# Performance work log

Measured on AMD Instinct MI355X. Metric: run time of the kernel, lower is better.

Reference implementation:

```python
import jax, jax.numpy as jnp
import numpy as np

NH, NP, C = 12, 4, 768           # heads, points, d_model
HD = C // NH                      # head dim (deform_ratio=1.0)
SHAPES = np.array([[128, 128], [64, 64], [32, 32]], dtype=np.int64)
LSI = np.array([0, 128 * 128, 128 * 128 + 64 * 64], dtype=np.int64)
L = SHAPES.shape[0]
EPS = 1e-6


def setup_inputs() -> dict:
    key = jax.random.key(0)
    ks = jax.random.split(key, 10)
    N, Lq = 4, 64 * 64
    Lin = int((SHAPES[:, 0] * SHAPES[:, 1]).sum())
    s = 0.02
    return {
        "query": jax.random.normal(ks[0], (N, Lq, C), jnp.float32),
        "reference_points": jax.random.uniform(ks[1], (N, Lq, L, 2), dtype=jnp.float32),
        "feat": jax.random.normal(ks[2], (N, Lin, C), jnp.float32),
        "qnorm_w": jnp.ones((C,), jnp.float32),
        "qnorm_b": jnp.zeros((C,), jnp.float32),
        "fnorm_w": jnp.ones((C,), jnp.float32),
        "fnorm_b": jnp.zeros((C,), jnp.float32),
        "gamma": jnp.full((C,), 0.01, jnp.float32),
        "so_w": s * jax.random.normal(ks[3], (C, NH * L * NP * 2), jnp.float32),
        "so_b": s * jax.random.normal(ks[4], (NH * L * NP * 2,), jnp.float32),
        "aw_w": s * jax.random.normal(ks[5], (C, NH * L * NP), jnp.float32),
        "aw_b": s * jax.random.normal(ks[6], (NH * L * NP,), jnp.float32),
        "vp_w": s * jax.random.normal(ks[7], (C, C), jnp.float32),
        "vp_b": jnp.zeros((C,), jnp.float32),
        "op_w": s * jax.random.normal(ks[8], (C, C), jnp.float32),
        "op_b": jnp.zeros((C,), jnp.float32),
        "spatial_shapes": SHAPES,
        "level_start_index": LSI,
    }


def _ln(x, w, b):
    mu = x.mean(-1, keepdims=True)
    var = ((x - mu) ** 2).mean(-1, keepdims=True)
    return (x - mu) * jax.lax.rsqrt(var + EPS) * w + b


def reference(query, reference_points, feat, qnorm_w, qnorm_b, fnorm_w, fnorm_b,
              gamma, so_w, so_b, aw_w, aw_b, vp_w, vp_b, op_w, op_b,
              spatial_shapes, level_start_index):
    N, Lq, C_ = query.shape
    ss = np.asarray(spatial_shapes)
    lsi = np.asarray(level_start_index)
    q = _ln(query, qnorm_w, qnorm_b)
    f = _ln(feat, fnorm_w, fnorm_b)
    # value projection -> [N, nh, Lin, hd]
    value = (f @ vp_w + vp_b).reshape(N, -1, NH, HD).transpose(0, 2, 1, 3)
    off = (q @ so_w + so_b).reshape(N, Lq, NH, L, NP, 2)
    aw = jax.nn.softmax((q @ aw_w + aw_b).reshape(N, Lq, NH, L * NP), axis=-1)
    aw = aw.reshape(N, Lq, NH, L, NP)
    # offset normalizer is (W, H) per level
    offset_norm = jnp.asarray(ss[:, ::-1].copy(), jnp.float32)
    loc = reference_points[:, :, None, :, None, :] + off / offset_norm[None, None, None, :, None, :]
    out = jnp.zeros((N, Lq, NH, HD), query.dtype)
    for l in range(L):
        H_, W_ = int(ss[l, 0]), int(ss[l, 1])
        st = int(lsi[l])
        v = value[:, :, st:st + H_ * W_, :]                     # [N,nh,HW,hd]
        ll = loc[:, :, :, l].transpose(0, 2, 1, 3, 4).reshape(N, NH, Lq * NP, 2)
        # grid_sample, align_corners=False: map [0,1] -> pixel coords
        px = ll[..., 0] * W_ - 0.5
        py = ll[..., 1] * H_ - 0.5
        x0 = jnp.floor(px)
        y0 = jnp.floor(py)
        tx = px - x0
        ty = py - y0
        x0i = x0.astype(jnp.int32)
        y0i = y0.astype(jnp.int32)
        acc = jnp.zeros((N, NH, Lq * NP, HD), query.dtype)
        for dx, dy, w in ((0, 0, (1 - tx) * (1 - ty)), (1, 0, tx * (1 - ty)),
                          (0, 1, (1 - tx) * ty), (1, 1, tx * ty)):
            xi = x0i + dx
            yi = y0i + dy
            ok = (xi >= 0) & (xi < W_) & (yi >= 0) & (yi < H_)  # zero padding
            idx = jnp.clip(yi, 0, H_ - 1) * W_ + jnp.clip(xi, 0, W_ - 1)
            g = jnp.take_along_axis(v, idx[..., None], axis=2)   # [N,nh,Lq*P,hd]
            acc = acc + g * (w * ok)[..., None]
        samp = acc.reshape(N, NH, Lq, NP, HD)
        out = out + jnp.einsum('nhqpd,nqhp->nqhd', samp, aw[:, :, :, l])
    attn = out.reshape(N, Lq, C_) @ op_w + op_b
    return query + gamma * attn
```

## Files before the change

### kernel.cpp

```cpp
#include <hip/hip_runtime.h>
#include <hip/hip_bf16.h>
#include <stdint.h>

#define NHD   12
#define NPT   4
#define CDIM  768
#define HDIM  64
#define NLVL  3
#define LQ    4096
#define NB    4
#define LIN   21504
#define MQ    (NB*LQ)
#define MF    (NB*LIN)
#define CAT_N 512
#define AW_OFF 288
#define WSCL  16.f
#define PREP_NB 1537

typedef float  f32x4  __attribute__((ext_vector_type(4)));
typedef float  f32x2  __attribute__((ext_vector_type(2)));
typedef float  f32x16 __attribute__((ext_vector_type(16)));
typedef int    i32x8  __attribute__((ext_vector_type(8)));

__device__ __forceinline__ i32x8 mk8(uint4 lo, uint4 hi) {
  i32x8 v;
  v[0] = (int)lo.x; v[1] = (int)lo.y; v[2] = (int)lo.z; v[3] = (int)lo.w;
  v[4] = (int)hi.x; v[5] = (int)hi.y; v[6] = (int)hi.z; v[7] = (int)hi.w;
  return v;
}

__global__ __launch_bounds__(256) void prep_and_ln(
    const float* __restrict__ vp_w, const float* __restrict__ op_w,
    const float* __restrict__ so_w, const float* __restrict__ aw_w,
    const float* __restrict__ so_b, const float* __restrict__ aw_b,
    char* __restrict__ vp_w8, char* __restrict__ op_w8,
    char* __restrict__ cat_w8, float* __restrict__ cat_bp,
    const float* __restrict__ xq, const float* __restrict__ wq,
    const float* __restrict__ bq, char* __restrict__ yq,
    const float* __restrict__ xf, const float* __restrict__ wf,
    const float* __restrict__ bf, char* __restrict__ yf)
{
  const int blk = blockIdx.x;
  if (blk >= PREP_NB) {
    const int lb = blk - PREP_NB;
    const float* x; const float* w; const float* b; char* y; int row;
    if (lb < MQ / 4) {
      x = xq; w = wq; b = bq; y = yq;
      row = lb * 4 + (threadIdx.x >> 6);
    } else {
      x = xf; w = wf; b = bf; y = yf;
      row = (lb - MQ / 4) * 4 + (threadIdx.x >> 6);
    }
    const int lane = threadIdx.x & 63;
    const float4* xr = (const float4*)(x + (size_t)row * CDIM);
    float4 v[3];
    v[0] = xr[lane]; v[1] = xr[lane + 64]; v[2] = xr[lane + 128];
    float s1 = 0.f, s2 = 0.f;
#pragma unroll
    for (int i = 0; i < 3; ++i) {
      s1 += v[i].x + v[i].y + v[i].z + v[i].w;
      s2 += v[i].x*v[i].x + v[i].y*v[i].y + v[i].z*v[i].z + v[i].w*v[i].w;
    }
#pragma unroll
    for (int o = 32; o > 0; o >>= 1) { s1 += __shfl_xor(s1, o); s2 += __shfl_xor(s2, o); }
    const float mu = s1 * (1.f / CDIM);
    const float rs = rsqrtf(s2 * (1.f / CDIM) - mu * mu + 1e-6f);
#pragma unroll
    for (int i = 0; i < 3; ++i) {
      const float4 w4 = ((const float4*)w)[lane + i * 64];
      const float4 b4 = ((const float4*)b)[lane + i * 64];
      const float o0 = (v[i].x - mu) * rs * w4.x + b4.x;
      const float o1 = (v[i].y - mu) * rs * w4.y + b4.y;
      const float o2 = (v[i].z - mu) * rs * w4.z + b4.z;
      const float o3 = (v[i].w - mu) * rs * w4.w + b4.w;
      uint32_t pk = 0;
      pk = __builtin_amdgcn_cvt_pk_fp8_f32(o0, o1, pk, false);
      pk = __builtin_amdgcn_cvt_pk_fp8_f32(o2, o3, pk, true);
      ((uint32_t*)(y + (size_t)row * CDIM))[lane + i * 64] = pk;
    }
    return;
  }
  const int b = blk;
  if (b == 1536) {
    const int i = threadIdx.x;
#pragma unroll
    for (int it = 0; it < 2; ++it) {
      const int idx = i + it * 256;
      float v = 0.f;
      if (idx < 288) v = so_b[idx];
      else if (idx < 432) v = aw_b[idx - AW_OFF];
      cat_bp[idx] = v;
    }
    return;
  }
  const float* W; char* Wt; int Nsrc, rowoff; float scale;
  int lb;
  if (b < 576)       { W = vp_w; Wt = vp_w8;  Nsrc = 768; rowoff = 0;   scale = 1.f;  lb = b; }
  else if (b < 1152) { W = op_w; Wt = op_w8;  Nsrc = 768; rowoff = 0;   scale = 1.f;  lb = b - 576; }
  else if (b < 1368) { W = so_w; Wt = cat_w8; Nsrc = 288; rowoff = 0;   scale = WSCL; lb = b - 1152; }
  else               { W = aw_w; Wt = cat_w8; Nsrc = 144; rowoff = 288; scale = WSCL; lb = b - 1368; }

  __shared__ float t[32][33];
  const int k0 = (lb % 24) * 32;
  const int n0 = (lb / 24) * 32;
  const int tx = threadIdx.x & 31, ty = threadIdx.x >> 5;
#pragma unroll
  for (int i = ty; i < 32; i += 8) {
    const int n = n0 + tx;
    t[i][tx] = (n < Nsrc) ? W[(size_t)(k0 + i) * Nsrc + n] * scale : 0.f;
  }
  __syncthreads();
#pragma unroll
  for (int i = ty; i < 32; i += 8) {
    const int n = rowoff + n0 + i;
    uint32_t pk = __builtin_amdgcn_cvt_pk_fp8_f32(t[tx][i], 0.f, 0, false);
    Wt[(size_t)n * CDIM + k0 + tx] = (char)(pk & 0xff);
  }
}

template<int MODE>
__global__ __launch_bounds__(256, 3) void gemm_mx(
    const char* __restrict__ A, const char* __restrict__ Wt,
    const float* __restrict__ bias, void* __restrict__ Cout,
    int M, int N, int K, int nTN, float oscale,
    const float* __restrict__ resid, const float* __restrict__ gammav)
{
  __shared__ __align__(16) char lds[49152];

  int bid = blockIdx.x;
  const int nwg = gridDim.x;
  if ((nwg & 7) == 0) {
    const int chunk = nwg >> 3;
    bid = (bid & 7) * chunk + (bid >> 3);
  }
  const int mt = bid / nTN, ntl = bid - mt * nTN;
  const int m0 = mt * 128, n0 = ntl * 128;
  const int tid  = threadIdx.x;
  const int lane = tid & 63, wid = tid >> 6;
  const int wm = wid >> 1, wn = wid & 1;
  const int lr31 = lane & 31, lkb = lane >> 5;

  f32x16 acc[2][2] = {};

  auto stage = [&](int kt, int buf, int ab) {
    const char* srcM = ab ? Wt : A;
    const int base0 = ab ? n0 : m0;
    const int k0 = kt * 64;
    char* dst0 = lds + buf * 16384 + ab * 8192;
#pragma unroll
    for (int it = 0; it < 2; ++it) {
      const int i = it * 256 + tid;
      const int r = i >> 2, p = i & 3;
      const int c = p ^ (r & 3);
      const char* src = srcM + (size_t)(base0 + r) * K + k0 + c * 16;
      char* dst = dst0 + (it * 256 + wid * 64) * 16;
      __builtin_amdgcn_global_load_lds(
          (const __attribute__((address_space(1))) uint32_t*)src,
          (__attribute__((address_space(3))) uint32_t*)dst, 16, 0, 0);
    }
  };
  auto rdop = [&](int buf, int ab, int row) -> i32x8 {
    const char* base = lds + buf * 16384 + ab * 8192 + row * 64;
    const int s = row & 3;
    const uint4 lo = *(const uint4*)(base + ((2 * lkb)     ^ s) * 16);
    const uint4 hi = *(const uint4*)(base + ((2 * lkb + 1) ^ s) * 16);
    return mk8(lo, hi);
  };

  const int nk = K >> 6;
  stage(0, 0, 0); stage(0, 0, 1);
  stage(1, 1, 0); stage(1, 1, 1);
  asm volatile("s_waitcnt vmcnt(4)" ::: "memory");
  __builtin_amdgcn_s_barrier();
  asm volatile("" ::: "memory");

  for (int t = 0; t < nk; ++t) {
    const int cur = t % 3;
    const i32x8 a0 = rdop(cur, 0, wm * 64 + lr31);
    const i32x8 a1 = rdop(cur, 0, wm * 64 + 32 + lr31);
    const i32x8 b0 = rdop(cur, 1, wn * 64 + lr31);
    const i32x8 b1 = rdop(cur, 1, wn * 64 + 32 + lr31);
    if (t + 2 < nk) { const int tb = (t + 2) % 3; stage(t + 2, tb, 0); stage(t + 2, tb, 1); }
    __builtin_amdgcn_s_setprio(1);
    acc[0][0] = __builtin_amdgcn_mfma_scale_f32_32x32x64_f8f6f4(
        a0, b0, acc[0][0], 0, 0, 0, 0x7F7F7F7F, 0, 0x7F7F7F7F);
    acc[0][1] = __builtin_amdgcn_mfma_scale_f32_32x32x64_f8f6f4(
        a0, b1, acc[0][1], 0, 0, 0, 0x7F7F7F7F, 0, 0x7F7F7F7F);
    acc[1][0] = __builtin_amdgcn_mfma_scale_f32_32x32x64_f8f6f4(
        a1, b0, acc[1][0], 0, 0, 0, 0x7F7F7F7F, 0, 0x7F7F7F7F);
    acc[1][1] = __builtin_amdgcn_mfma_scale_f32_32x32x64_f8f6f4(
        a1, b1, acc[1][1], 0, 0, 0, 0x7F7F7F7F, 0, 0x7F7F7F7F);
    __builtin_amdgcn_s_setprio(0);
    if (t + 2 < nk)      asm volatile("s_waitcnt vmcnt(4)" ::: "memory");
    else if (t + 1 < nk) asm volatile("s_waitcnt vmcnt(0)" ::: "memory");
    __builtin_amdgcn_s_barrier();
    asm volatile("" ::: "memory");
  }

  if constexpr (MODE == 0) {
    const int head  = (n0 + wn * 64) >> 6;
    const int n_img = (unsigned)m0 / LIN;
    char* plane = (char*)Cout + ((size_t)(n_img * NHD + head) * LIN
                                 + (m0 - n_img * LIN)) * 64;
    float bcol[2];
#pragma unroll
    for (int nt2 = 0; nt2 < 2; ++nt2)
      bcol[nt2] = bias[n0 + wn * 64 + nt2 * 32 + lr31];
    float* my = (float*)(lds + wid * 8704);
#pragma unroll
    for (int mt2 = 0; mt2 < 2; ++mt2) {
#pragma unroll
      for (int nt2 = 0; nt2 < 2; ++nt2)
#pragma unroll
        for (int reg = 0; reg < 16; ++reg) {
          const int row = (reg & 3) + 8 * (reg >> 2) + 4 * lkb;
          my[row * 68 + nt2 * 32 + lr31] = acc[mt2][nt2][reg] + bcol[nt2];
        }
#pragma unroll
      for (int it = 0; it < 2; ++it) {
        const int idx = it * 64 + lane;
        const int row = idx >> 2, seg = idx & 3;
        const float* s = my + row * 68 + seg * 16;
        uint32_t w[4];
#pragma unroll
        for (int q = 0; q < 4; ++q) {
          uint32_t pk = 0;
          pk = __builtin_amdgcn_cvt_pk_fp8_f32(s[q*4+0], s[q*4+1], pk, false);
          pk = __builtin_amdgcn_cvt_pk_fp8_f32(s[q*4+2], s[q*4+3], pk, true);
          w[q] = pk;
        }
        char* orow = plane + (size_t)(wm * 64 + mt2 * 32 + row) * 64 + seg * 16;
        *(uint4*)orow = *(uint4*)w;
      }
    }
  } else {
#pragma unroll
    for (int nt2 = 0; nt2 < 2; ++nt2) {
      const int col = n0 + wn * 64 + nt2 * 32 + lr31;
      const float bcol = bias[col];
      float gcol = 0.f;
      if constexpr (MODE == 2) gcol = gammav[col];
#pragma unroll
      for (int mt2 = 0; mt2 < 2; ++mt2)
#pragma unroll
        for (int reg = 0; reg < 16; ++reg) {
          const int row = m0 + wm * 64 + mt2 * 32
                        + (reg & 3) + 8 * (reg >> 2) + 4 * lkb;
          const size_t o = (size_t)row * N + col;
          if constexpr (MODE == 1)
            ((float*)Cout)[o] = acc[mt2][nt2][reg] * oscale + bcol;
          else
            ((float*)Cout)[o] = resid[o] + gcol * (acc[mt2][nt2][reg] + bcol);
        }
    }
  }
}

__global__ __launch_bounds__(256) void deform_fused(
    const char* __restrict__ vbytes, const float* __restrict__ raw,
    const float* __restrict__ refp, char* __restrict__ samp)
{
  const int j = blockIdx.x;
  const int x = j & 7, k = j >> 3;
  const int g = x + ((k >> 6) << 3);
  const int i = k & 63;
  const int n = g / NHD, h = g - n * NHD;
  const int q0 = i * 64;

  __shared__ float4 pp_lds[64][12];

  if (threadIdx.x < 64) {
    const int nq = n * LQ + q0 + threadIdx.x;
    const float* praw = raw + (size_t)nq * CAT_N;
    float v[12], m = -1e30f;
#pragma unroll
    for (int jj = 0; jj < 12; ++jj) {
      v[jj] = praw[AW_OFF + h * 12 + jj];
      m = fmaxf(m, v[jj]);
    }
    float s = 0.f;
#pragma unroll
    for (int jj = 0; jj < 12; ++jj) { v[jj] = __expf(v[jj] - m); s += v[jj]; }
    const float inv = 1.f / s;
    const float* op = praw + h * 24;
    const float* rp = refp + (size_t)nq * (NLVL * 2);
    const float Wf[3] = {128.f, 64.f, 32.f};
#pragma unroll
    for (int l = 0; l < NLVL; ++l) {
      const float rxw = rp[2 * l] * Wf[l] - 0.5f;
      const float ryw = rp[2 * l + 1] * Wf[l] - 0.5f;
#pragma unroll
      for (int pt = 0; pt < NPT; ++pt) {
        float4 o4;
        o4.x = rxw + op[(l * 4 + pt) * 2 + 0];
        o4.y = ryw + op[(l * 4 + pt) * 2 + 1];
        o4.z = v[l * 4 + pt] * inv;
        o4.w = 0.f;
        pp_lds[threadIdx.x][l * 4 + pt] = o4;
      }
    }
  }
  __syncthreads();

  const int wid = threadIdx.x >> 6, lane = threadIdx.x & 63;
  const int qi = lane >> 2, ci = lane & 3;
  const int ql = wid * 16 + qi;
  const int nq = n * LQ + q0 + ql;
  const float4* __restrict__ pp = pp_lds[ql];
  const uint32_t base0 = (uint32_t)g * (uint32_t)(LIN * 64)
                       + ((uint32_t)ci << 4);

  float acc[16];
#pragma unroll
  for (int c = 0; c < 16; ++c) acc[c] = 0.f;

  const int      Wl[3]  = {128, 64, 32};
  const uint32_t STb[3] = {0u, 16384u * 64u, 20480u * 64u};

#pragma unroll
  for (int l = 0; l < NLVL; ++l) {
    const int W_ = Wl[l];
    const uint32_t base = base0 + STb[l];
#pragma unroll
    for (int p = 0; p < NPT; ++p) {
      const float4 pt = pp[l * 4 + p];
      const float fx = floorf(pt.x), fy = floorf(pt.y);
      const float tx = pt.x - fx,   ty = pt.y - fy;
      const int x0 = (int)fx, y0 = (int)fy;
      const int x1 = x0 + 1,  y1 = y0 + 1;
      const float wx0 = ((uint32_t)x0 < (uint32_t)W_) ? (1.f - tx) : 0.f;
      const float wx1 = ((uint32_t)x1 < (uint32_t)W_) ? tx : 0.f;
      const float wy0 = ((uint32_t)y0 < (uint32_t)W_) ? pt.z * (1.f - ty) : 0.f;
      const float wy1 = ((uint32_t)y1 < (uint32_t)W_) ? pt.z * ty : 0.f;
      const int xc0 = min(max(x0, 0), W_ - 1);
      const int xc1 = min(max(x1, 0), W_ - 1);
      const int yr0 = min(max(y0, 0), W_ - 1) * W_;
      const int yr1 = min(max(y1, 0), W_ - 1) * W_;
      const float cw[4] = {wy0 * wx0, wy0 * wx1, wy1 * wx0, wy1 * wx1};
      const uint4 G0 = *(const uint4*)(vbytes + base + (uint32_t)(yr0 + xc0) * 64u);
      const uint4 G1 = *(const uint4*)(vbytes + base + (uint32_t)(yr0 + xc1) * 64u);
      const uint4 G2 = *(const uint4*)(vbytes + base + (uint32_t)(yr1 + xc0) * 64u);
      const uint4 G3 = *(const uint4*)(vbytes + base + (uint32_t)(yr1 + xc1) * 64u);
      const uint4 GG[4] = {G0, G1, G2, G3};
#pragma unroll
      for (int cnr = 0; cnr < 4; ++cnr) {
        const uint32_t wds[4] = {GG[cnr].x, GG[cnr].y, GG[cnr].z, GG[cnr].w};
        const float wgt = cw[cnr];
#pragma unroll
        for (int wd = 0; wd < 4; ++wd) {
          f32x2 lo = __builtin_amdgcn_cvt_pk_f32_fp8(wds[wd], false);
          f32x2 hi = __builtin_amdgcn_cvt_pk_f32_fp8(wds[wd], true);
          acc[wd * 4 + 0] += lo[0] * wgt;
          acc[wd * 4 + 1] += lo[1] * wgt;
          acc[wd * 4 + 2] += hi[0] * wgt;
          acc[wd * 4 + 3] += hi[1] * wgt;
        }
      }
    }
  }

  uint32_t out[4];
#pragma unroll
  for (int wd = 0; wd < 4; ++wd) {
    uint32_t pk = 0;
    pk = __builtin_amdgcn_cvt_pk_fp8_f32(acc[wd*4+0], acc[wd*4+1], pk, false);
    pk = __builtin_amdgcn_cvt_pk_fp8_f32(acc[wd*4+2], acc[wd*4+3], pk, true);
    out[wd] = pk;
  }
  *(uint4*)(samp + (size_t)nq * CDIM + h * HDIM + ci * 16) = *(uint4*)out;
}

extern "C" void kernel_launch(void* const* d_in, const int* in_sizes, int n_in,
                              void* d_out, int out_size, void* d_ws, size_t ws_size,
                              hipStream_t stream) {
  const float* query = (const float*)d_in[0];
  const float* refp  = (const float*)d_in[1];
  const float* feat  = (const float*)d_in[2];
  const float* qn_w  = (const float*)d_in[3];
  const float* qn_b  = (const float*)d_in[4];
  const float* fn_w  = (const float*)d_in[5];
  const float* fn_b  = (const float*)d_in[6];
  const float* gamma = (const float*)d_in[7];
  const float* so_w  = (const float*)d_in[8];
  const float* so_b  = (const float*)d_in[9];
  const float* aw_w  = (const float*)d_in[10];
  const float* aw_b  = (const float*)d_in[11];
  const float* vp_w  = (const float*)d_in[12];
  const float* vp_b  = (const float*)d_in[13];
  const float* op_w  = (const float*)d_in[14];
  const float* op_b  = (const float*)d_in[15];

  char* ws = (char*)d_ws;
  size_t off = 0;
  auto alloc = [&](size_t bytes) {
    char* p = ws + off;
    off = (off + bytes + 255) & ~(size_t)255;
    return p;
  };
  char*   q_f8   = (char*)alloc((size_t)MQ * CDIM);
  char*   val_f8 = (char*)alloc((size_t)MF * CDIM);
  char*   vp_w8  = (char*)alloc((size_t)CDIM * CDIM);
  char*   op_w8  = (char*)alloc((size_t)CDIM * CDIM);
  char*   cat_w8 = (char*)alloc((size_t)CAT_N * CDIM);
  float*  cat_bp = (float*)alloc(CAT_N * 4);

  const size_t r = off;
  char* f_f8 = ws + r;
  const size_t f_end = r + (size_t)MF * CDIM;
  size_t o2 = r;
  float*  raw     = (float*)(ws + o2);  o2 += (size_t)MQ * CAT_N * 4;
  char*   samp8   = (char*)(ws + o2);   o2 += (size_t)MQ * CDIM;
  const size_t need = (f_end > o2) ? f_end : o2;
  if (ws_size < need) return;

  prep_and_ln<<<PREP_NB + (MQ + MF) / 4, 256, 0, stream>>>(
      vp_w, op_w, so_w, aw_w, so_b, aw_b, vp_w8, op_w8, cat_w8, cat_bp,
      query, qn_w, qn_b, q_f8, feat, fn_w, fn_b, f_f8);

  gemm_mx<0><<<(MF / 128) * (CDIM / 128), 256, 0, stream>>>(
      f_f8, vp_w8, vp_b, val_f8, MF, CDIM, CDIM, CDIM / 128,
      1.f, nullptr, nullptr);

  gemm_mx<1><<<(MQ / 128) * (CAT_N / 128), 256, 0, stream>>>(
      q_f8, cat_w8, cat_bp, raw, MQ, CAT_N, CDIM, CAT_N / 128,
      1.f / WSCL, nullptr, nullptr);

  deform_fused<<<48 * 64, 256, 0, stream>>>(val_f8, raw, refp, samp8);

  gemm_mx<2><<<(MQ / 128) * (CDIM / 128), 256, 0, stream>>>(
      samp8, op_w8, op_b, (float*)d_out, MQ, CDIM, CDIM, CDIM / 128,
      1.f, query, gamma);
}
```

Baseline: 240.0 us.

## Merge value and offset GEMMs into one launch; parallelize deform softmax prep

The value-projection GEMM and the offset/attention-weight GEMM are combined into a single grid, with blocks dispatched by index. This removes one launch and fills the tail of the larger GEMM with work from the smaller one. The output GEMM becomes a dedicated kernel with constant dimensions. In the deform kernel, the per-query softmax and sampling-location setup is now spread over all 256 threads, four per query using shuffle reductions, instead of only the first 64 threads. The merged kernel adds a runtime mode branch and may cost some registers.

```diff
diff --git a/kernel.cpp b/kernel.cpp
--- a/kernel.cpp
+++ b/kernel.cpp
@@ -16,6 +16,8 @@
 #define AW_OFF 288
 #define WSCL  16.f
 #define PREP_NB 1537
+#define VAL_NWG ((MF/128)*(CDIM/128))
+#define CAT_NWG ((MQ/128)*(CAT_N/128))
 
 typedef float  f32x4  __attribute__((ext_vector_type(4)));
 typedef float  f32x2  __attribute__((ext_vector_type(2)));
@@ -118,19 +120,27 @@
   }
 }
 
-template<int MODE>
-__global__ __launch_bounds__(256, 3) void gemm_mx(
-    const char* __restrict__ A, const char* __restrict__ Wt,
-    const float* __restrict__ bias, void* __restrict__ Cout,
-    int M, int N, int K, int nTN, float oscale,
-    const float* __restrict__ resid, const float* __restrict__ gammav)
+__global__ __launch_bounds__(256, 3) void gemm_dual(
+    const char* __restrict__ A0, const char* __restrict__ W0,
+    const float* __restrict__ b0, char* __restrict__ C0,
+    const char* __restrict__ A1, const char* __restrict__ W1,
+    const float* __restrict__ b1, float* __restrict__ C1, float oscale1)
 {
   __shared__ __align__(16) char lds[49152];
 
   int bid = blockIdx.x;
-  const int nwg = gridDim.x;
-  if ((nwg & 7) == 0) {
-    const int chunk = nwg >> 3;
+  int mode, nTN;
+  const char* A; const char* Wt; const float* bias;
+  if (bid < VAL_NWG) {
+    mode = 0; nTN = CDIM / 128;
+    A = A0; Wt = W0; bias = b0;
+    const int chunk = VAL_NWG >> 3;
+    bid = (bid & 7) * chunk + (bid >> 3);
+  } else {
+    mode = 1; nTN = CAT_N / 128;
+    A = A1; Wt = W1; bias = b1;
+    bid -= VAL_NWG;
+    const int chunk = CAT_NWG >> 3;
     bid = (bid & 7) * chunk + (bid >> 3);
   }
   const int mt = bid / nTN, ntl = bid - mt * nTN;
@@ -139,6 +149,136 @@
   const int lane = tid & 63, wid = tid >> 6;
   const int wm = wid >> 1, wn = wid & 1;
   const int lr31 = lane & 31, lkb = lane >> 5;
+  const int K = CDIM;
+
+  f32x16 acc[2][2] = {};
+
+  auto stage = [&](int kt, int buf, int ab) {
+    const char* srcM = ab ? Wt : A;
+    const int base0 = ab ? n0 : m0;
+    const int k0 = kt * 64;
+    char* dst0 = lds + buf * 16384 + ab * 8192;
+#pragma unroll
+    for (int it = 0; it < 2; ++it) {
+      const int i = it * 256 + tid;
+      const int r = i >> 2, p = i & 3;
+      const int c = p ^ (r & 3);
+      const char* src = srcM + (size_t)(base0 + r) * K + k0 + c * 16;
+      char* dst = dst0 + (it * 256 + wid * 64) * 16;
+      __builtin_amdgcn_global_load_lds(
+          (const __attribute__((address_space(1))) uint32_t*)src,
+          (__attribute__((address_space(3))) uint32_t*)dst, 16, 0, 0);
+    }
+  };
+  auto rdop = [&](int buf, int ab, int row) -> i32x8 {
+    const char* base = lds + buf * 16384 + ab * 8192 + row * 64;
+    const int s = row & 3;
+    const uint4 lo = *(const uint4*)(base + ((2 * lkb)     ^ s) * 16);
+    const uint4 hi = *(const uint4*)(base + ((2 * lkb + 1) ^ s) * 16);
+    return mk8(lo, hi);
+  };
+
+  const int nk = K >> 6;
+  stage(0, 0, 0); stage(0, 0, 1);
+  stage(1, 1, 0); stage(1, 1, 1);
+  asm volatile("s_waitcnt vmcnt(4)" ::: "memory");
+  __builtin_amdgcn_s_barrier();
+  asm volatile("" ::: "memory");
+
+  for (int t = 0; t < nk; ++t) {
+    const int cur = t % 3;
+    const i32x8 a0 = rdop(cur, 0, wm * 64 + lr31);
+    const i32x8 a1 = rdop(cur, 0, wm * 64 + 32 + lr31);
+    const i32x8 b0v = rdop(cur, 1, wn * 64 + lr31);
+    const i32x8 b1v = rdop(cur, 1, wn * 64 + 32 + lr31);
+    if (t + 2 < nk) { const int tb = (t + 2) % 3; stage(t + 2, tb, 0); stage(t + 2, tb, 1); }
+    __builtin_amdgcn_s_setprio(1);
+    acc[0][0] = __builtin_amdgcn_mfma_scale_f32_32x32x64_f8f6f4(
+        a0, b0v, acc[0][0], 0, 0, 0, 0x7F7F7F7F, 0, 0x7F7F7F7F);
+    acc[0][1] = __builtin_amdgcn_mfma_scale_f32_32x32x64_f8f6f4(
+        a0, b1v, acc[0][1], 0, 0, 0, 0x7F7F7F7F, 0, 0x7F7F7F7F);
+    acc[1][0] = __builtin_amdgcn_mfma_scale_f32_32x32x64_f8f6f4(
+        a1, b0v, acc[1][0], 0, 0, 0, 0x7F7F7F7F, 0, 0x7F7F7F7F);
+    acc[1][1] = __builtin_amdgcn_mfma_scale_f32_32x32x64_f8f6f4(
+        a1, b1v, acc[1][1], 0, 0, 0, 0x7F7F7F7F, 0, 0x7F7F7F7F);
+    __builtin_amdgcn_s_setprio(0);
+    if (t + 2 < nk)      asm volatile("s_waitcnt vmcnt(4)" ::: "memory");
+    else if (t + 1 < nk) asm volatile("s_waitcnt vmcnt(0)" ::: "memory");
+    __builtin_amdgcn_s_barrier();
+    asm volatile("" ::: "memory");
+  }
+
+  if (mode == 0) {
+    const int head  = (n0 + wn * 64) >> 6;
+    const int n_img = (unsigned)m0 / LIN;
+    char* plane = C0 + ((size_t)(n_img * NHD + head) * LIN
+                        + (m0 - n_img * LIN)) * 64;
+    float bcol[2];
+#pragma unroll
+    for (int nt2 = 0; nt2 < 2; ++nt2)
+      bcol[nt2] = bias[n0 + wn * 64 + nt2 * 32 + lr31];
+    float* my = (float*)(lds + wid * 8704);
+#pragma unroll
+    for (int mt2 = 0; mt2 < 2; ++mt2) {
+#pragma unroll
+      for (int nt2 = 0; nt2 < 2; ++nt2)
+#pragma unroll
+        for (int reg = 0; reg < 16; ++reg) {
+          const int row = (reg & 3) + 8 * (reg >> 2) + 4 * lkb;
+          my[row * 68 + nt2 * 32 + lr31] = acc[mt2][nt2][reg] + bcol[nt2];
+        }
+#pragma unroll
+      for (int it = 0; it < 2; ++it) {
+        const int idx = it * 64 + lane;
+        const int row = idx >> 2, seg = idx & 3;
+        const float* s = my + row * 68 + seg * 16;
+        uint32_t w[4];
+#pragma unroll
+        for (int q = 0; q < 4; ++q) {
+          uint32_t pk = 0;
+          pk = __builtin_amdgcn_cvt_pk_fp8_f32(s[q*4+0], s[q*4+1], pk, false);
+          pk = __builtin_amdgcn_cvt_pk_fp8_f32(s[q*4+2], s[q*4+3], pk, true);
+          w[q] = pk;
+        }
+        char* orow = plane + (size_t)(wm * 64 + mt2 * 32 + row) * 64 + seg * 16;
+        *(uint4*)orow = *(uint4*)w;
+      }
+    }
+  } else {
+#pragma unroll
+    for (int nt2 = 0; nt2 < 2; ++nt2) {
+      const int col = n0 + wn * 64 + nt2 * 32 + lr31;
+      const float bcol = bias[col];
+#pragma unroll
+      for (int mt2 = 0; mt2 < 2; ++mt2)
+#pragma unroll
+        for (int reg = 0; reg < 16; ++reg) {
+          const int row = m0 + wm * 64 + mt2 * 32
+                        + (reg & 3) + 8 * (reg >> 2) + 4 * lkb;
+          C1[(size_t)row * CAT_N + col] = acc[mt2][nt2][reg] * oscale1 + bcol;
+        }
+    }
+  }
+}
+
+__global__ __launch_bounds__(256, 3) void gemm_op(
+    const char* __restrict__ A, const char* __restrict__ Wt,
+    const float* __restrict__ bias, float* __restrict__ Cout,
+    const float* __restrict__ resid, const float* __restrict__ gammav)
+{
+  __shared__ __align__(16) char lds[49152];
+
+  int bid = blockIdx.x;
+  const int nwg = gridDim.x;
+  { const int chunk = nwg >> 3; bid = (bid & 7) * chunk + (bid >> 3); }
+  const int nTN = CDIM / 128;
+  const int mt = bid / nTN, ntl = bid - mt * nTN;
+  const int m0 = mt * 128, n0 = ntl * 128;
+  const int tid  = threadIdx.x;
+  const int lane = tid & 63, wid = tid >> 6;
+  const int wm = wid >> 1, wn = wid & 1;
+  const int lr31 = lane & 31, lkb = lane >> 5;
+  const int K = CDIM;
 
   f32x16 acc[2][2] = {};
 
@@ -197,62 +337,20 @@
     asm volatile("" ::: "memory");
   }
 
-  if constexpr (MODE == 0) {
-    const int head  = (n0 + wn * 64) >> 6;
-    const int n_img = (unsigned)m0 / LIN;
-    char* plane = (char*)Cout + ((size_t)(n_img * NHD + head) * LIN
-                                 + (m0 - n_img * LIN)) * 64;
-    float bcol[2];
-#pragma unroll
-    for (int nt2 = 0; nt2 < 2; ++nt2)
-      bcol[nt2] = bias[n0 + wn * 64 + nt2 * 32 + lr31];
-    float* my = (float*)(lds + wid * 8704);
-#pragma unroll
-    for (int mt2 = 0; mt2 < 2; ++mt2) {
-#pragma unroll
-      for (int nt2 = 0; nt2 < 2; ++nt2)
-#pragma unroll
-        for (int reg = 0; reg < 16; ++reg) {
-          const int row = (reg & 3) + 8 * (reg >> 2) + 4 * lkb;
-          my[row * 68 + nt2 * 32 + lr31] = acc[mt2][nt2][reg] + bcol[nt2];
-        }
-#pragma unroll
-      for (int it = 0; it < 2; ++it) {
-        const int idx = it * 64 + lane;
-        const int row = idx >> 2, seg = idx & 3;
-        const float* s = my + row * 68 + seg * 16;
-        uint32_t w[4];
-#pragma unroll
-        for (int q = 0; q < 4; ++q) {
-          uint32_t pk = 0;
-          pk = __builtin_amdgcn_cvt_pk_fp8_f32(s[q*4+0], s[q*4+1], pk, false);
-          pk = __builtin_amdgcn_cvt_pk_fp8_f32(s[q*4+2], s[q*4+3], pk, true);
-          w[q] = pk;
-        }
-        char* orow = plane + (size_t)(wm * 64 + mt2 * 32 + row) * 64 + seg * 16;
-        *(uint4*)orow = *(uint4*)w;
+#pragma unroll
+  for (int nt2 = 0; nt2 < 2; ++nt2) {
+    const int col = n0 + wn * 64 + nt2 * 32 + lr31;
+    const float bcol = bias[col];
+    const float gcol = gammav[col];
+#pragma unroll
+    for (int mt2 = 0; mt2 < 2; ++mt2)
+#pragma unroll
+      for (int reg = 0; reg < 16; ++reg) {
+        const int row = m0 + wm * 64 + mt2 * 32
+                      + (reg & 3) + 8 * (reg >> 2) + 4 * lkb;
+        const size_t o = (size_t)row * CDIM + col;
+        Cout[o] = resid[o] + gcol * (acc[mt2][nt2][reg] + bcol);
       }
-    }
-  } else {
-#pragma unroll
-    for (int nt2 = 0; nt2 < 2; ++nt2) {
-      const int col = n0 + wn * 64 + nt2 * 32 + lr31;
-      const float bcol = bias[col];
-      float gcol = 0.f;
-      if constexpr (MODE == 2) gcol = gammav[col];
-#pragma unroll
-      for (int mt2 = 0; mt2 < 2; ++mt2)
-#pragma unroll
-        for (int reg = 0; reg < 16; ++reg) {
-          const int row = m0 + wm * 64 + mt2 * 32
-                        + (reg & 3) + 8 * (reg >> 2) + 4 * lkb;
-          const size_t o = (size_t)row * N + col;
-          if constexpr (MODE == 1)
-            ((float*)Cout)[o] = acc[mt2][nt2][reg] * oscale + bcol;
-          else
-            ((float*)Cout)[o] = resid[o] + gcol * (acc[mt2][nt2][reg] + bcol);
-        }
-    }
   }
 }
 
@@ -269,35 +367,38 @@
 
   __shared__ float4 pp_lds[64][12];
 
-  if (threadIdx.x < 64) {
-    const int nq = n * LQ + q0 + threadIdx.x;
+  {
+    const int ql = threadIdx.x >> 2;
+    const int s  = threadIdx.x & 3;
+    const int nq = n * LQ + q0 + ql;
     const float* praw = raw + (size_t)nq * CAT_N;
-    float v[12], m = -1e30f;
-#pragma unroll
-    for (int jj = 0; jj < 12; ++jj) {
-      v[jj] = praw[AW_OFF + h * 12 + jj];
+    float v[3], m = -1e30f;
+#pragma unroll
+    for (int jj = 0; jj < 3; ++jj) {
+      v[jj] = praw[AW_OFF + h * 12 + s * 3 + jj];
       m = fmaxf(m, v[jj]);
     }
-    float s = 0.f;
-#pragma unroll
-    for (int jj = 0; jj < 12; ++jj) { v[jj] = __expf(v[jj] - m); s += v[jj]; }
-    const float inv = 1.f / s;
+    m = fmaxf(m, __shfl_xor(m, 1));
+    m = fmaxf(m, __shfl_xor(m, 2));
+    float sum = 0.f;
+#pragma unroll
+    for (int jj = 0; jj < 3; ++jj) { v[jj] = __expf(v[jj] - m); sum += v[jj]; }
+    sum += __shfl_xor(sum, 1);
+    sum += __shfl_xor(sum, 2);
+    const float inv = 1.f / sum;
     const float* op = praw + h * 24;
     const float* rp = refp + (size_t)nq * (NLVL * 2);
-    const float Wf[3] = {128.f, 64.f, 32.f};
-#pragma unroll
-    for (int l = 0; l < NLVL; ++l) {
-      const float rxw = rp[2 * l] * Wf[l] - 0.5f;
-      const float ryw = rp[2 * l + 1] * Wf[l] - 0.5f;
-#pragma unroll
-      for (int pt = 0; pt < NPT; ++pt) {
-        float4 o4;
-        o4.x = rxw + op[(l * 4 + pt) * 2 + 0];
-        o4.y = ryw + op[(l * 4 + pt) * 2 + 1];
-        o4.z = v[l * 4 + pt] * inv;
-        o4.w = 0.f;
-        pp_lds[threadIdx.x][l * 4 + pt] = o4;
-      }
+#pragma unroll
+    for (int jj = 0; jj < 3; ++jj) {
+      const int jd = s * 3 + jj;
+      const int l = jd >> 2;
+      const float Wf = (float)(128 >> l);
+      float4 o4;
+      o4.x = rp[2 * l] * Wf - 0.5f + op[jd * 2 + 0];
+      o4.y = rp[2 * l + 1] * Wf - 0.5f + op[jd * 2 + 1];
+      o4.z = v[jj] * inv;
+      o4.w = 0.f;
+      pp_lds[ql][jd] = o4;
     }
   }
   __syncthreads();
@@ -417,17 +518,12 @@
       vp_w, op_w, so_w, aw_w, so_b, aw_b, vp_w8, op_w8, cat_w8, cat_bp,
       query, qn_w, qn_b, q_f8, feat, fn_w, fn_b, f_f8);
 
-  gemm_mx<0><<<(MF / 128) * (CDIM / 128), 256, 0, stream>>>(
-      f_f8, vp_w8, vp_b, val_f8, MF, CDIM, CDIM, CDIM / 128,
-      1.f, nullptr, nullptr);
-
-  gemm_mx<1><<<(MQ / 128) * (CAT_N / 128), 256, 0, stream>>>(
-      q_f8, cat_w8, cat_bp, raw, MQ, CAT_N, CDIM, CAT_N / 128,
-      1.f / WSCL, nullptr, nullptr);
+  gemm_dual<<<VAL_NWG + CAT_NWG, 256, 0, stream>>>(
+      f_f8, vp_w8, vp_b, val_f8,
+      q_f8, cat_w8, cat_bp, raw, 1.f / WSCL);
 
   deform_fused<<<48 * 64, 256, 0, stream>>>(val_f8, raw, refp, samp8);
 
-  gemm_mx<2><<<(MQ / 128) * (CDIM / 128), 256, 0, stream>>>(
-      samp8, op_w8, op_b, (float*)d_out, MQ, CDIM, CDIM, CDIM / 128,
-      1.f, query, gamma);
+  gemm_op<<<(MQ / 128) * (CDIM / 128), 256, 0, stream>>>(
+      samp8, op_w8, op_b, (float*)d_out, query, gamma);
 }
```

New measurement: 236.8 us. No clear change (-1.3%).
